# Performance work log

Measured on AMD Instinct MI355X. Metric: run time of the kernel, lower is better.

Reference implementation:

```python
import jax, jax.numpy as jnp
import numpy as np

N_NODES = 50000
N_EDGES = 800000
HIDDEN = 256
N_LAYERS = 3
N_PAIRS = 4096


def setup_inputs() -> dict:
    key = jax.random.key(0)
    ks = jax.random.split(key, 10)
    s = 1.0 / np.sqrt(HIDDEN)
    x = jax.random.normal(ks[0], (N_NODES, HIDDEN), dtype=jnp.float32)
    f0_w = jax.random.normal(ks[1], (N_LAYERS, HIDDEN, HIDDEN), dtype=jnp.float32) * s
    f0_b = jax.random.normal(ks[2], (N_LAYERS, HIDDEN), dtype=jnp.float32) * s
    f1_w = jax.random.normal(ks[3], (N_LAYERS, HIDDEN, HIDDEN), dtype=jnp.float32) * s
    f1_b = jax.random.normal(ks[4], (N_LAYERS, HIDDEN), dtype=jnp.float32) * s
    conv_w = jax.random.normal(ks[5], (N_LAYERS, HIDDEN, HIDDEN), dtype=jnp.float32) * s
    conv_b = jax.random.normal(ks[6], (N_LAYERS, HIDDEN), dtype=jnp.float32) * s
    edge_src = jax.random.randint(ks[7], (N_EDGES,), 0, N_NODES, dtype=jnp.int64 if jax.config.jax_enable_x64 else jnp.int32)
    edge_dst = jax.random.randint(ks[8], (N_EDGES,), 0, N_NODES, dtype=edge_src.dtype)
    pos = jax.random.randint(ks[9], (N_PAIRS, 2), 0, N_NODES, dtype=edge_src.dtype)
    return {"x": x, "f0_w": f0_w, "f0_b": f0_b, "f1_w": f1_w, "f1_b": f1_b,
            "conv_w": conv_w, "conv_b": conv_b,
            "edge_src": edge_src, "edge_dst": edge_dst, "pos": pos}


def reference(x, f0_w, f0_b, f1_w, f1_b, conv_w, conv_b, edge_src, edge_dst, pos):
    # Faithful translation of FLabelingNet.forward:
    #   for each layer: x0 = f0(x); x0[idx] = f1(x[idx]); x = conv(x0, adj)
    #   return x[pos]
    n = x.shape[0]
    idx = pos.reshape(-1)  # (2M,) labeled node indices
    for i in range(f0_w.shape[0]):
        x0 = x @ f0_w[i] + f0_b[i]                       # (N, F) elementwise linear
        lbl = x[idx] @ f1_w[i] + f1_b[i]                 # (2M, F) transform of labeled rows
        x0 = x0.at[idx].set(lbl)                         # scatter-overwrite selected rows
        h = x0 @ conv_w[i] + conv_b[i]                   # node-wise linear of the conv
        # sparse adjacency message passing: out[v] = sum_{(u,v) in E} h[u]
        x = jax.ops.segment_sum(h[edge_src], edge_dst, num_segments=n)
    return x[pos]  # (M, 2, F)
```

## Files before the change

### kernel.cpp

```cpp
#include <hip/hip_runtime.h>
#include <hip/hip_bf16.h>

#define N_NODES 50000
#define N_EDGES 800000
#define HIDDEN  256
#define N_LAYERS 3
#define N_PAIRS 4096
#define N_LABEL 8192
#define NPAD    50176
#define SCAN_BLOCKS (NPAD / 256)
#define WSZ (HIDDEN * HIDDEN)

#define NROWPAD (N_NODES + 1)
#define SLICE_ELEMS ((size_t)NROWPAD * 32)
#define SEG_CHUNKS ((N_NODES + 63) / 64)

typedef __bf16 bf16x8 __attribute__((ext_vector_type(8)));
typedef __bf16 bf16x4 __attribute__((ext_vector_type(4)));
typedef float  f32x4  __attribute__((ext_vector_type(4)));
typedef float  f32x2  __attribute__((ext_vector_type(2)));

__device__ __forceinline__ void load_lds16(const void* g, void* l) {
    __builtin_amdgcn_global_load_lds(
        (const __attribute__((address_space(1))) void*)g,
        (__attribute__((address_space(3))) void*)l, 16, 0, 0);
}

__device__ __forceinline__ void acc8(const uint4 w, f32x2* a) {
    a[0] += (f32x2){__uint_as_float(w.x << 16), __uint_as_float(w.x & 0xffff0000u)};
    a[1] += (f32x2){__uint_as_float(w.y << 16), __uint_as_float(w.y & 0xffff0000u)};
    a[2] += (f32x2){__uint_as_float(w.z << 16), __uint_as_float(w.z & 0xffff0000u)};
    a[3] += (f32x2){__uint_as_float(w.w << 16), __uint_as_float(w.w & 0xffff0000u)};
}

template <bool DEG_BIAS, bool A_FP32>
__global__ __launch_bounds__(256) void mfma_gemm_fused(
    const void* __restrict__ A_in,
    const __bf16* __restrict__ Wt0, const __bf16* __restrict__ Wt1,
    const float* __restrict__ bD0, const float* __restrict__ bD1,
    const float* __restrict__ bC0, const float* __restrict__ bC1,
    __bf16* __restrict__ Cout,
    const int* __restrict__ idx,
    const int* __restrict__ degv,
    const int* __restrict__ flags,
    int M)
{
    const int role = blockIdx.z;
    if (role == 1 && blockIdx.x >= N_LABEL / 64) return;

    const __bf16* A   = (const __bf16*)A_in;
    const float*  A32 = (const float*)A_in;
    const __bf16* Wt  = role ? Wt1 : Wt0;
    const float*  bD  = role ? bD1 : bD0;
    const float*  bC  = role ? bC1 : bC0;

    __shared__ __bf16 As[64 * 32];
    __shared__ __bf16 Bs[128 * 32];
    __shared__ int s_idx[64];

    const int t    = threadIdx.x;
    const int lane = t & 63;
    const int wave = t >> 6;
    const int m0   = blockIdx.x * 64;
    const int n0   = blockIdx.y * 128;

    if (role == 1) {
        if (t < 64) s_idx[t] = idx[m0 + t];
        __syncthreads();
    }

    const int arow  = t >> 2;
    const int acol8 = (t & 3) * 8;
    int anode;
    if (role == 1) {
        anode = s_idx[arow];
    } else {
        const int rg = m0 + arow;
        anode = (rg < M) ? rg : (M - 1);
    }
    const __bf16* aptr   = A   + (size_t)anode * HIDDEN + acol8;
    const float*  aptr32 = A32 + (size_t)anode * HIDDEN + acol8;

    const __bf16* bptr[2];
    #pragma unroll
    for (int r = 0; r < 2; ++r) {
        const int c = r * 256 + t;
        bptr[r] = Wt + (size_t)(n0 + (c >> 2)) * HIDDEN + (c & 3) * 8;
    }

    f32x4 acc[8];
    #pragma unroll
    for (int i = 0; i < 8; ++i) acc[i] = (f32x4){0.f, 0.f, 0.f, 0.f};

    const int wm   = wave * 16;
    const int fm   = lane & 15;
    const int quad = lane >> 4;

    for (int k0 = 0; k0 < HIDDEN; k0 += 32) {
        __syncthreads();
        if constexpr (A_FP32) {
            const float* ap = aptr32 + k0;
            const float4 u0 = *(const float4*)(ap);
            const float4 u1 = *(const float4*)(ap + 4);
            bf16x8 w = {(__bf16)u0.x, (__bf16)u0.y, (__bf16)u0.z, (__bf16)u0.w,
                        (__bf16)u1.x, (__bf16)u1.y, (__bf16)u1.z, (__bf16)u1.w};
            *(bf16x8*)(As + (size_t)t * 8) = w;
        } else {
            load_lds16(aptr + k0, (void*)(As + (size_t)t * 8));
        }
        #pragma unroll
        for (int r = 0; r < 2; ++r)
            load_lds16(bptr[r] + k0, (void*)(Bs + (size_t)(r * 256 + t) * 8));
        __syncthreads();

        const bf16x8 af = *(const bf16x8*)(As + (wm + fm) * 32 + quad * 8);
        bf16x8 bfr[8];
        #pragma unroll
        for (int nt = 0; nt < 8; ++nt)
            bfr[nt] = *(const bf16x8*)(Bs + (nt * 16 + fm) * 32 + quad * 8);

        #pragma unroll
        for (int nt = 0; nt < 8; ++nt)
            acc[nt] = __builtin_amdgcn_mfma_f32_16x16x32_bf16(
                af, bfr[nt], acc[nt], 0, 0, 0);
    }

    float bd[8], bc[8];
    #pragma unroll
    for (int nt = 0; nt < 8; ++nt) {
        const int col = n0 + nt * 16 + fm;
        bd[nt] = DEG_BIAS ? bD[col] : 0.f;
        bc[nt] = bC[col];
    }

    #pragma unroll
    for (int rg = 0; rg < 4; ++rg) {
        const int rloc = wm + quad * 4 + rg;
        int orow;
        if (role == 1) {
            orow = s_idx[rloc];
        } else {
            orow = m0 + rloc;
            if (orow >= M) continue;
            if (flags[orow]) continue;
        }
        float bscale = 0.f;
        if constexpr (DEG_BIAS)
            bscale = (float)degv[orow];
        #pragma unroll
        for (int nt = 0; nt < 8; ++nt) {
            const int cb = n0 + nt * 16;
            float v = acc[nt][rg];
            if constexpr (DEG_BIAS) v += bscale * bd[nt];
            v += bc[nt];
            Cout[(size_t)(cb >> 5) * SLICE_ELEMS + (size_t)orow * 32
                 + (cb & 31) + fm] = (__bf16)v;
        }
    }
}

template <bool GATHER_A, bool DEG_BIAS, bool DEG_VIA_IDX, bool OUT_BF16, bool PROD_BATCH>
__global__ __launch_bounds__(256) void mfma_gemm(
    const __bf16* __restrict__ A_in,
    const __bf16* __restrict__ Wt_in,
    const float* __restrict__ biasD,
    void* __restrict__ Cout_in,
    const int* __restrict__ idx,
    const int* __restrict__ degv,
    int M)
{
    const __bf16* A  = A_in;
    const __bf16* Wt = Wt_in;
    void* Cout = Cout_in;
    if constexpr (PROD_BATCH) {
        const int z = blockIdx.z;
        A    = A_in  + (size_t)(3 * (1 + (z >> 1)) + (z & 1)) * WSZ;
        Wt   = Wt_in + (size_t)(z >> 1) * WSZ;
        Cout = (void*)((__bf16*)Cout_in + (size_t)z * WSZ);
    }

    __shared__ __bf16 As[64 * 32];
    __shared__ __bf16 Bs[128 * 32];
    __shared__ int s_idx[64];

    const int t    = threadIdx.x;
    const int lane = t & 63;
    const int wave = t >> 6;
    const int m0   = blockIdx.x * 64;
    const int n0   = blockIdx.y * 128;

    if constexpr (GATHER_A || DEG_VIA_IDX) {
        if (t < 64) s_idx[t] = idx[m0 + t];
        __syncthreads();
    }

    const int arow  = t >> 2;
    const int acol8 = (t & 3) * 8;
    int anode;
    if constexpr (GATHER_A) {
        anode = s_idx[arow];
    } else {
        const int rg = m0 + arow;
        anode = (rg < M) ? rg : (M - 1);
    }
    const __bf16* aptr = A + (size_t)anode * HIDDEN + acol8;

    const __bf16* bptr[2];
    #pragma unroll
    for (int r = 0; r < 2; ++r) {
        const int c = r * 256 + t;
        bptr[r] = Wt + (size_t)(n0 + (c >> 2)) * HIDDEN + (c & 3) * 8;
    }

    f32x4 acc[8];
    #pragma unroll
    for (int i = 0; i < 8; ++i) acc[i] = (f32x4){0.f, 0.f, 0.f, 0.f};

    const int wm   = wave * 16;
    const int fm   = lane & 15;
    const int quad = lane >> 4;

    for (int k0 = 0; k0 < HIDDEN; k0 += 32) {
        __syncthreads();
        load_lds16(aptr + k0, (void*)(As + (size_t)t * 8));
        #pragma unroll
        for (int r = 0; r < 2; ++r)
            load_lds16(bptr[r] + k0, (void*)(Bs + (size_t)(r * 256 + t) * 8));
        __syncthreads();

        const bf16x8 af = *(const bf16x8*)(As + (wm + fm) * 32 + quad * 8);
        bf16x8 bfr[8];
        #pragma unroll
        for (int nt = 0; nt < 8; ++nt)
            bfr[nt] = *(const bf16x8*)(Bs + (nt * 16 + fm) * 32 + quad * 8);

        #pragma unroll
        for (int nt = 0; nt < 8; ++nt)
            acc[nt] = __builtin_amdgcn_mfma_f32_16x16x32_bf16(
                af, bfr[nt], acc[nt], 0, 0, 0);
    }

    float bd[8];
    #pragma unroll
    for (int nt = 0; nt < 8; ++nt)
        bd[nt] = DEG_BIAS ? biasD[n0 + nt * 16 + fm] : 0.f;

    #pragma unroll
    for (int rg = 0; rg < 4; ++rg) {
        const int rloc = wm + quad * 4 + rg;
        const int orow = m0 + rloc;
        if (!PROD_BATCH && orow >= M) continue;
        int dnode = orow;
        if constexpr (GATHER_A || DEG_VIA_IDX) dnode = s_idx[rloc];
        float bscale = 0.f;
        if constexpr (DEG_BIAS)
            bscale = (float)degv[dnode];
        #pragma unroll
        for (int nt = 0; nt < 8; ++nt) {
            const int col = n0 + nt * 16 + fm;
            float v = acc[nt][rg];
            if constexpr (DEG_BIAS) v += bscale * bd[nt];
            if constexpr (OUT_BF16)
                ((__bf16*)Cout)[(size_t)orow * HIDDEN + col] = (__bf16)v;
            else
                ((float*)Cout)[(size_t)orow * HIDDEN + col] = v;
        }
    }
}

__global__ __launch_bounds__(256) void wconv_kernel(
    const float* __restrict__ f0_w, const float* __restrict__ f1_w,
    const float* __restrict__ conv_w, const float* __restrict__ conv_b,
    __bf16* __restrict__ wt_all, __bf16* __restrict__ cw_nt,
    float* __restrict__ q)
{
    const int z = blockIdx.z;
    const int kx = blockIdx.x * 32, nx = blockIdx.y * 32;
    const int tx = threadIdx.x, ty = threadIdx.y;

    if (z < 9) {
        const int layer = z / 3, which = z % 3;
        const float* W = ((which == 0) ? f0_w : (which == 1) ? f1_w : conv_w)
                         + (size_t)layer * WSZ;
        __bf16* T = wt_all + (size_t)z * WSZ;

        __shared__ float tile[32][33];
        for (int i = ty; i < 32; i += 8)
            tile[i][tx] = W[(size_t)(kx + i) * HIDDEN + nx + tx];
        __syncthreads();
        for (int i = ty; i < 32; i += 8)
            T[(size_t)(nx + i) * HIDDEN + kx + tx] = (__bf16)tile[tx][i];
    } else if (z < 11) {
        const int layer = z - 9;
        const float* W = conv_w + (size_t)layer * WSZ;
        __bf16* T = cw_nt + (size_t)layer * WSZ;
        for (int i = ty; i < 32; i += 8)
            T[(size_t)(kx + i) * HIDDEN + nx + tx] =
                (__bf16)W[(size_t)(kx + i) * HIDDEN + nx + tx];
    } else {
        if (blockIdx.x >= 4 || blockIdx.y != 0) return;
        const int zq = blockIdx.x;
        const int l = zq >> 1, branch = zq & 1;
        const float* cb = conv_b + (size_t)l * HIDDEN;
        const float* W  = (branch ? f1_w : f0_w) + (size_t)(l + 1) * WSZ;
        const int n = ty * 32 + tx;
        float s = 0.f;
        #pragma unroll 4
        for (int k = 0; k < HIDDEN; ++k)
            s += cb[k] * W[(size_t)k * HIDDEN + n];
        q[(size_t)zq * HIDDEN + n] = s;
    }
}

__global__ __launch_bounds__(256) void hist_kernel(
    const int* __restrict__ dst, const int* __restrict__ pos,
    int* __restrict__ counts, int* __restrict__ flags,
    __bf16* __restrict__ x0b)
{
    int e = blockIdx.x * 256 + threadIdx.x;
    if (e < N_EDGES) atomicAdd(&counts[dst[e]], 1);
    if (e < N_LABEL) flags[pos[e]] = 1;
    if (blockIdx.x == 0) {
        const int sl = threadIdx.x >> 5, c = threadIdx.x & 31;
        x0b[(size_t)sl * SLICE_ELEMS + (size_t)N_NODES * 32 + c] = (__bf16)0.f;
    }
}

__device__ __forceinline__ int block_incl_scan(int v, int* s, int t)
{
    s[t] = v; __syncthreads();
    #pragma unroll
    for (int off = 1; off < 256; off <<= 1) {
        int add = (t >= off) ? s[t - off] : 0;
        __syncthreads();
        s[t] += add;
        __syncthreads();
    }
    return s[t];
}

__global__ __launch_bounds__(256) void scan1_kernel(
    const int* __restrict__ counts, int* __restrict__ offs, int* __restrict__ bsum)
{
    __shared__ int s[256];
    const int t = threadIdx.x;
    const int i = blockIdx.x * 256 + t;
    const int pv = (counts[i] + 7) & ~7;
    int incl = block_incl_scan(pv, s, t);
    offs[i] = incl - pv;
    if (t == 255) bsum[blockIdx.x] = incl;
}

__global__ __launch_bounds__(256) void scan2_kernel(
    const int* __restrict__ bsum, int* __restrict__ bbase)
{
    __shared__ int s[256];
    const int t = threadIdx.x;
    const int v = (t < SCAN_BLOCKS) ? bsum[t] : 0;
    int incl = block_incl_scan(v, s, t);
    bbase[t] = incl - v;
}

__global__ __launch_bounds__(256) void scan3_kernel(
    int* __restrict__ offs, const int* __restrict__ bbase,
    int* __restrict__ cursor, const int* __restrict__ counts,
    int* __restrict__ src_sorted)
{
    const int i = blockIdx.x * 256 + threadIdx.x;
    const int o = offs[i] + bbase[blockIdx.x];
    offs[i] = o;
    cursor[i] = o;
    const int v  = counts[i];
    const int pv = (v + 7) & ~7;
    for (int j = o + v; j < o + pv; ++j) src_sorted[j] = N_NODES;
}

__global__ __launch_bounds__(256) void fill_kernel(
    const int* __restrict__ src, const int* __restrict__ dst,
    int* __restrict__ cursor, int* __restrict__ src_sorted)
{
    int e = blockIdx.x * 256 + threadIdx.x;
    if (e < N_EDGES) {
        int p = atomicAdd(&cursor[dst[e]], 1);
        src_sorted[p] = src[e];
    }
}

template <bool COMPACT>
__global__ __launch_bounds__(256) void seg_slice_kernel(
    const __bf16* __restrict__ x0b,
    const int* __restrict__ srcs,
    const int* __restrict__ offs,
    const int* __restrict__ nodelist,
    __bf16* __restrict__ out)
{
    const int slice = blockIdx.x & 7;
    const int chunk = blockIdx.x >> 3;
    const int t    = threadIdx.x;
    const int wave = t >> 6;
    const int lane = t & 63;
    const int g    = lane >> 2;
    const int li   = lane & 3;
    const int rw   = chunk * 64 + wave * 16 + g;
    if (!COMPACT && rw >= N_NODES) return;

    const int d    = COMPACT ? nodelist[rw] : rw;
    const int beg  = offs[d];
    const int pdeg = offs[d + 1] - beg;

    const char* xb = (const char*)(x0b + (size_t)slice * SLICE_ELEMS);
    const uint32_t lioff = (uint32_t)li * 16u;
    const int* sp = srcs + beg;

    f32x2 a[4];
    #pragma unroll
    for (int j = 0; j < 4; ++j) a[j] = (f32x2){0.f, 0.f};

    int4 j0, j1;
    if (pdeg > 0) {
        j0 = *(const int4*)(sp);
        j1 = *(const int4*)(sp + 4);
    }

    for (int base = 0; base < pdeg; base += 8) {
        const int4 k0 = j0, k1 = j1;
        if (base + 8 < pdeg) {
            j0 = *(const int4*)(sp + base + 8);
            j1 = *(const int4*)(sp + base + 12);
        }
        const uint4 c0 = *(const uint4*)(xb + (((uint32_t)k0.x << 6) + lioff));
        const uint4 c1 = *(const uint4*)(xb + (((uint32_t)k0.y << 6) + lioff));
        const uint4 c2 = *(const uint4*)(xb + (((uint32_t)k0.z << 6) + lioff));
        const uint4 c3 = *(const uint4*)(xb + (((uint32_t)k0.w << 6) + lioff));
        const uint4 c4 = *(const uint4*)(xb + (((uint32_t)k1.x << 6) + lioff));
        const uint4 c5 = *(const uint4*)(xb + (((uint32_t)k1.y << 6) + lioff));
        const uint4 c6 = *(const uint4*)(xb + (((uint32_t)k1.z << 6) + lioff));
        const uint4 c7 = *(const uint4*)(xb + (((uint32_t)k1.w << 6) + lioff));
        acc8(c0, a); acc8(c1, a); acc8(c2, a); acc8(c3, a);
        acc8(c4, a); acc8(c5, a); acc8(c6, a); acc8(c7, a);
    }

    bf16x8 o;
    #pragma unroll
    for (int j = 0; j < 4; ++j) {
        o[2 * j]     = (__bf16)a[j].x;
        o[2 * j + 1] = (__bf16)a[j].y;
    }
    *(bf16x8*)(out + (size_t)rw * HIDDEN + (slice << 5) + li * 8) = o;
}

extern "C" void kernel_launch(void* const* d_in, const int* in_sizes, int n_in,
                              void* d_out, int out_size, void* d_ws, size_t ws_size,
                              hipStream_t stream)
{
    const float* x       = (const float*)d_in[0];
    const float* f0_w    = (const float*)d_in[1];
    const float* f0_b    = (const float*)d_in[2];
    const float* f1_w    = (const float*)d_in[3];
    const float* f1_b    = (const float*)d_in[4];
    const float* conv_w  = (const float*)d_in[5];
    const float* conv_b  = (const float*)d_in[6];
    const int*   edge_src = (const int*)d_in[7];
    const int*   edge_dst = (const int*)d_in[8];
    const int*   pos      = (const int*)d_in[9];
    float* out = (float*)d_out;

    const size_t buf = (size_t)N_NODES * HIDDEN;

    char* p = (char*)d_ws;
    __bf16* bufA   = (__bf16*)p; p += buf * 2;
    __bf16* bufB   = (__bf16*)p; p += SLICE_ELEMS * 8 * 2;
    __bf16* s_lbl  = (__bf16*)p; p += (size_t)N_LABEL * HIDDEN * 2;
    __bf16* wt_all = (__bf16*)p; p += (size_t)9 * WSZ * 2;
    __bf16* prod   = (__bf16*)p; p += (size_t)4 * WSZ * 2;
    __bf16* cw_nt  = (__bf16*)p; p += (size_t)2 * WSZ * 2;
    float*  qv     = (float*)p;  p += (size_t)4 * HIDDEN * 4;
    int* counts     = (int*)p;  p += NPAD * 4;
    int* flags      = (int*)p;  p += NPAD * 4;
    int* offs       = (int*)p;  p += NPAD * 4;
    int* cursor     = (int*)p;  p += NPAD * 4;
    int* bsum       = (int*)p;  p += 256 * 4;
    int* bbase      = (int*)p;  p += 256 * 4;
    int* src_sorted = (int*)p;  p += (size_t)(N_EDGES + 7 * NPAD) * 4;

    const int edge_blocks = (N_EDGES + 255) / 256;

    hipMemsetAsync(counts, 0, 2 * NPAD * sizeof(int), stream);
    hist_kernel<<<edge_blocks, 256, 0, stream>>>(edge_dst, pos, counts, flags, bufB);
    scan1_kernel<<<SCAN_BLOCKS, 256, 0, stream>>>(counts, offs, bsum);
    scan2_kernel<<<1, 256, 0, stream>>>(bsum, bbase);
    scan3_kernel<<<SCAN_BLOCKS, 256, 0, stream>>>(offs, bbase, cursor, counts, src_sorted);
    fill_kernel<<<edge_blocks, 256, 0, stream>>>(edge_src, edge_dst, cursor, src_sorted);

    wconv_kernel<<<dim3(8, 8, 12), dim3(32, 8), 0, stream>>>(
        f0_w, f1_w, conv_w, conv_b, wt_all, cw_nt, qv);

    mfma_gemm<false, false, false, true, true><<<dim3(4, 2, 4), 256, 0, stream>>>(
        wt_all, cw_nt, nullptr, prod, nullptr, nullptr, HIDDEN);

    const dim3 fused_grid(782, 2, 2);
    const dim3 lbl_grid(128, 2);

    __bf16* cur = bufA;
    __bf16* tmp = bufB;

    for (int l = 0; l < N_LAYERS; ++l) {
        const float* B0 = f0_b + (size_t)l * HIDDEN;
        const float* B1 = f1_b + (size_t)l * HIDDEN;

        if (l == 0) {
            mfma_gemm_fused<false, true><<<fused_grid, 256, 0, stream>>>(
                x, wt_all + 0 * WSZ, wt_all + 1 * WSZ,
                nullptr, nullptr, B0, B1, tmp, pos, counts, flags, N_NODES);
        } else {
            const int z0 = (l - 1) * 2;
            mfma_gemm_fused<true, false><<<fused_grid, 256, 0, stream>>>(
                cur, prod + (size_t)z0 * WSZ, prod + (size_t)(z0 + 1) * WSZ,
                qv + (size_t)z0 * HIDDEN, qv + (size_t)(z0 + 1) * HIDDEN,
                B0, B1, tmp, pos, counts, flags, N_NODES);
        }

        if (l < N_LAYERS - 1) {
            seg_slice_kernel<false><<<8 * SEG_CHUNKS, 256, 0, stream>>>(
                tmp, src_sorted, offs, nullptr, cur);
        } else {
            seg_slice_kernel<true><<<8 * (N_LABEL / 64), 256, 0, stream>>>(
                tmp, src_sorted, offs, pos, s_lbl);
            mfma_gemm<false, true, true, false, false><<<lbl_grid, 256, 0, stream>>>(
                s_lbl, wt_all + (size_t)(2 * 3 + 2) * WSZ,
                conv_b + (size_t)2 * HIDDEN, out, pos, counts, N_LABEL);
        }
    }
}
```

Before: 389.5 us.

## Fold histogram into weight-convert kernel and edge fill into first GEMM

Removes the standalone histogram and CSR fill kernels. The degree histogram now runs as extra z-planes of the weight-conversion launch, and the edge bucket fill runs as a third role of the layer-0 fused GEMM grid. This cuts two kernel launches and lets the atomic-heavy preprocessing overlap with the weight transpose and the first GEMM. The cost is a larger grid with idle or divergent blocks and mixed workloads contending in the same launch.

```diff
diff --git a/kernel.cpp b/kernel.cpp
--- a/kernel.cpp
+++ b/kernel.cpp
@@ -43,9 +43,26 @@
     const int* __restrict__ idx,
     const int* __restrict__ degv,
     const int* __restrict__ flags,
+    const int* __restrict__ esrc,
+    const int* __restrict__ edst,
+    int* __restrict__ cursor,
+    int* __restrict__ ssorted,
     int M)
 {
     const int role = blockIdx.z;
+    if (role == 2) {
+        const int eb = blockIdx.x * 2 + blockIdx.y;
+        int e = eb * 512 + threadIdx.x;
+        #pragma unroll
+        for (int r = 0; r < 2; ++r) {
+            if (e < N_EDGES) {
+                const int p = atomicAdd(&cursor[edst[e]], 1);
+                ssorted[p] = esrc[e];
+            }
+            e += 256;
+        }
+        return;
+    }
     if (role == 1 && blockIdx.x >= N_LABEL / 64) return;
 
     const __bf16* A   = (const __bf16*)A_in;
@@ -272,11 +289,29 @@
     const float* __restrict__ f0_w, const float* __restrict__ f1_w,
     const float* __restrict__ conv_w, const float* __restrict__ conv_b,
     __bf16* __restrict__ wt_all, __bf16* __restrict__ cw_nt,
-    float* __restrict__ q)
+    float* __restrict__ q,
+    const int* __restrict__ edge_dst, const int* __restrict__ pos,
+    int* __restrict__ counts, int* __restrict__ flags,
+    __bf16* __restrict__ x0b)
 {
     const int z = blockIdx.z;
+    const int tx = threadIdx.x, ty = threadIdx.y;
+
+    if (z >= 12) {
+        const int plane = z - 12;
+        const int t = ty * 32 + tx;
+        const int eb = plane * 64 + blockIdx.x * 8 + blockIdx.y;
+        const int e = eb * 256 + t;
+        if (e < N_EDGES) atomicAdd(&counts[edge_dst[e]], 1);
+        if (e < N_LABEL) flags[pos[e]] = 1;
+        if (plane == 0 && blockIdx.x == 0 && blockIdx.y == 0) {
+            const int sl = t >> 5, c = t & 31;
+            x0b[(size_t)sl * SLICE_ELEMS + (size_t)N_NODES * 32 + c] = (__bf16)0.f;
+        }
+        return;
+    }
+
     const int kx = blockIdx.x * 32, nx = blockIdx.y * 32;
-    const int tx = threadIdx.x, ty = threadIdx.y;
 
     if (z < 9) {
         const int layer = z / 3, which = z % 3;
@@ -312,20 +347,6 @@
     }
 }
 
-__global__ __launch_bounds__(256) void hist_kernel(
-    const int* __restrict__ dst, const int* __restrict__ pos,
-    int* __restrict__ counts, int* __restrict__ flags,
-    __bf16* __restrict__ x0b)
-{
-    int e = blockIdx.x * 256 + threadIdx.x;
-    if (e < N_EDGES) atomicAdd(&counts[dst[e]], 1);
-    if (e < N_LABEL) flags[pos[e]] = 1;
-    if (blockIdx.x == 0) {
-        const int sl = threadIdx.x >> 5, c = threadIdx.x & 31;
-        x0b[(size_t)sl * SLICE_ELEMS + (size_t)N_NODES * 32 + c] = (__bf16)0.f;
-    }
-}
-
 __device__ __forceinline__ int block_incl_scan(int v, int* s, int t)
 {
     s[t] = v; __syncthreads();
@@ -373,17 +394,6 @@
     const int v  = counts[i];
     const int pv = (v + 7) & ~7;
     for (int j = o + v; j < o + pv; ++j) src_sorted[j] = N_NODES;
-}
-
-__global__ __launch_bounds__(256) void fill_kernel(
-    const int* __restrict__ src, const int* __restrict__ dst,
-    int* __restrict__ cursor, int* __restrict__ src_sorted)
-{
-    int e = blockIdx.x * 256 + threadIdx.x;
-    if (e < N_EDGES) {
-        int p = atomicAdd(&cursor[dst[e]], 1);
-        src_sorted[p] = src[e];
-    }
 }
 
 template <bool COMPACT>
@@ -483,21 +493,18 @@
     int* bbase      = (int*)p;  p += 256 * 4;
     int* src_sorted = (int*)p;  p += (size_t)(N_EDGES + 7 * NPAD) * 4;
 
-    const int edge_blocks = (N_EDGES + 255) / 256;
-
     hipMemsetAsync(counts, 0, 2 * NPAD * sizeof(int), stream);
-    hist_kernel<<<edge_blocks, 256, 0, stream>>>(edge_dst, pos, counts, flags, bufB);
+    wconv_kernel<<<dim3(8, 8, 61), dim3(32, 8), 0, stream>>>(
+        f0_w, f1_w, conv_w, conv_b, wt_all, cw_nt, qv,
+        edge_dst, pos, counts, flags, bufB);
     scan1_kernel<<<SCAN_BLOCKS, 256, 0, stream>>>(counts, offs, bsum);
     scan2_kernel<<<1, 256, 0, stream>>>(bsum, bbase);
     scan3_kernel<<<SCAN_BLOCKS, 256, 0, stream>>>(offs, bbase, cursor, counts, src_sorted);
-    fill_kernel<<<edge_blocks, 256, 0, stream>>>(edge_src, edge_dst, cursor, src_sorted);
-
-    wconv_kernel<<<dim3(8, 8, 12), dim3(32, 8), 0, stream>>>(
-        f0_w, f1_w, conv_w, conv_b, wt_all, cw_nt, qv);
 
     mfma_gemm<false, false, false, true, true><<<dim3(4, 2, 4), 256, 0, stream>>>(
         wt_all, cw_nt, nullptr, prod, nullptr, nullptr, HIDDEN);
 
+    const dim3 fused_grid0(782, 2, 3);
     const dim3 fused_grid(782, 2, 2);
     const dim3 lbl_grid(128, 2);
 
@@ -509,15 +516,17 @@
         const float* B1 = f1_b + (size_t)l * HIDDEN;
 
         if (l == 0) {
-            mfma_gemm_fused<false, true><<<fused_grid, 256, 0, stream>>>(
+            mfma_gemm_fused<false, true><<<fused_grid0, 256, 0, stream>>>(
                 x, wt_all + 0 * WSZ, wt_all + 1 * WSZ,
-                nullptr, nullptr, B0, B1, tmp, pos, counts, flags, N_NODES);
+                nullptr, nullptr, B0, B1, tmp, pos, counts, flags,
+                edge_src, edge_dst, cursor, src_sorted, N_NODES);
         } else {
             const int z0 = (l - 1) * 2;
             mfma_gemm_fused<true, false><<<fused_grid, 256, 0, stream>>>(
                 cur, prod + (size_t)z0 * WSZ, prod + (size_t)(z0 + 1) * WSZ,
                 qv + (size_t)z0 * HIDDEN, qv + (size_t)(z0 + 1) * HIDDEN,
-                B0, B1, tmp, pos, counts, flags, N_NODES);
+                B0, B1, tmp, pos, counts, flags,
+                nullptr, nullptr, nullptr, nullptr, N_NODES);
         }
 
         if (l < N_LAYERS - 1) {
```

New measurement: 395.3 us. No clear change (+1.5%).
